# Optimization experiments

Hardware: AMD Instinct MI355X
Metric: run time of the kernel (lower is better)

## Reference

```python
import jax, jax.numpy as jnp
import numpy as np

QMIN, QMAX = -128.0, 127.0  # int8 fake-quant range for activations
BIAS_ZP = 128.0             # zero point for the uint8-stored quantized bias


def ste_fake_quant(x, scale, zp):
    # scaled fake-quantize: q = clip(round(x/s) + zp, qmin, qmax); deq = (q - zp) * s
    q = jnp.clip(jnp.round(x / scale) + zp, QMIN, QMAX)
    deq = (q - zp) * scale
    # straight-through estimator (matches torch fake_quantize semantics)
    return x + jax.lax.stop_gradient(deq - x)


def setup_inputs() -> dict:
    key = jax.random.key(0)
    ks = jax.random.split(key, 8)
    B, S, K, N, G = 8, 8192, 1024, 1024, 128
    NG = K // G  # groups per output channel
    x = jax.random.normal(ks[0], (B, S, K), dtype=jnp.float32)
    w_q = jax.random.randint(ks[1], (N, K), 0, 16, dtype=jnp.int32)          # int4 codes
    w_scale = jax.random.uniform(ks[2], (N, NG), dtype=jnp.float32) * 0.02 + 1e-3
    w_zp = jax.random.randint(ks[3], (N, NG), 0, 16, dtype=jnp.int32)
    bias_q = jax.random.randint(ks[4], (N,), 0, 256, dtype=jnp.int32)        # uint8 codes
    bias_scale = jax.random.uniform(ks[5], (N,), dtype=jnp.float32) * 0.01 + 1e-4
    in_scale = jax.random.uniform(ks[6], (1,), dtype=jnp.float32) * 0.02 + 0.01
    in_zp = jnp.zeros((1,), dtype=jnp.int32)
    out_scale = jax.random.uniform(ks[7], (1,), dtype=jnp.float32) * 0.2 + 0.05
    out_zp = jnp.zeros((1,), dtype=jnp.int32)
    return {"x": x, "w_q": w_q, "w_scale": w_scale, "w_zp": w_zp,
            "bias_q": bias_q, "bias_scale": bias_scale,
            "in_scale": in_scale, "in_zp": in_zp,
            "out_scale": out_scale, "out_zp": out_zp}


def reference(x, w_q, w_scale, w_zp, bias_q, bias_scale, in_scale, in_zp, out_scale, out_zp):
    dt = x.dtype
    N, K = w_q.shape
    NG = w_scale.shape[1]
    G = K // NG
    # group-wise weight dequantize: [N, K] -> [N, NG, G]
    wq = w_q.reshape(N, NG, G).astype(dt)
    W = ((wq - w_zp[:, :, None].astype(dt)) * w_scale[:, :, None].astype(dt)).reshape(N, K)
    # per-channel bias dequantize
    bias = (bias_q.astype(dt) - BIAS_ZP) * bias_scale.astype(dt)
    # per-tensor fake-quantize of the input activation
    xq = ste_fake_quant(x, in_scale.astype(dt), in_zp.astype(dt))
    # func_method: linear
    out = jnp.einsum('bsk,nk->bsn', xq, W) + bias
    # per-tensor fake-quantize of the output
    return ste_fake_quant(out, out_scale.astype(dt), out_zp.astype(dt))
```

## Files before the change

kernel.cpp:

```cpp
#include <hip/hip_runtime.h>
#include <hip/hip_bf16.h>
#include <stdint.h>

#define M_DIM 65536
#define K_DIM 1024
#define N_DIM 1024
#define NGRP  8

#define NIT 8

#define FB_BM 128
#define FB_BN 128
#define FB_BK 32
#define FB_NKT (K_DIM / FB_BK)

typedef float f32x4 __attribute__((ext_vector_type(4)));
typedef int   ix4   __attribute__((ext_vector_type(4)));
typedef __bf16 bf16x8 __attribute__((ext_vector_type(8)));

__global__ void prep_wd_kernel(const int* __restrict__ w_q,
                               const int* __restrict__ w_zp,
                               const int* __restrict__ bias_q,
                               const float* __restrict__ bias_scale,
                               int8_t* __restrict__ Wd,
                               float* __restrict__ bias_f) {
    const int n = blockIdx.x;
    const int t = threadIdx.x;
    const int k0 = t * 4;
    const int g = k0 >> 7;
    const int zp = w_zp[n * NGRP + g];
    const int4 wq = *reinterpret_cast<const int4*>(w_q + (size_t)n * K_DIM + k0);
    union { int u; int8_t b[4]; } pk;
    pk.b[0] = (int8_t)(wq.x - zp);
    pk.b[1] = (int8_t)(wq.y - zp);
    pk.b[2] = (int8_t)(wq.z - zp);
    pk.b[3] = (int8_t)(wq.w - zp);
    *reinterpret_cast<int*>(Wd + (size_t)n * K_DIM + k0) = pk.u;
    if (t == 0) bias_f[n] = ((float)bias_q[n] - 128.0f) * bias_scale[n];
}

__global__ __launch_bounds__(256) void prep_x8_kernel(
    const float* __restrict__ x,
    const float* __restrict__ in_scale_p, const int* __restrict__ in_zp_p,
    int8_t* __restrict__ Xq)
{
    const float s = in_scale_p[0];
    const float inv = 1.0f / s;
    const float zp = (float)in_zp_p[0];
    const size_t i = ((size_t)blockIdx.x * 256 + threadIdx.x) * 16;
    float vv[16];
#pragma unroll
    for (int c = 0; c < 4; ++c) {
        const float4 v = *reinterpret_cast<const float4*>(x + i + c * 4);
        vv[c * 4 + 0] = v.x; vv[c * 4 + 1] = v.y;
        vv[c * 4 + 2] = v.z; vv[c * 4 + 3] = v.w;
    }
    union { int4 u; int8_t b[16]; } pk;
#pragma unroll
    for (int e = 0; e < 16; ++e) {
        float q = rintf(vv[e] * inv) + zp;
        q = fminf(fmaxf(q, -128.0f), 127.0f);
        pk.b[e] = (int8_t)(q - zp);
    }
    *reinterpret_cast<int4*>(Xq + i) = pk.u;
}

__global__ __launch_bounds__(512, 2) void gemm256_i8_kernel(
    const int8_t* __restrict__ Xq,
    const int8_t* __restrict__ Wd,
    const float* __restrict__ w_scale,
    const float* __restrict__ bias_f,
    const float* __restrict__ in_scale_p,
    const float* __restrict__ out_scale_p, const int* __restrict__ out_zp_p,
    float* __restrict__ out)
{
    __shared__ __align__(16) int8_t LDS[8][16384];
    __shared__ float WS[NGRP * 256];

    const int t = threadIdx.x;
    const int bid = (blockIdx.x & 7) * 128 + (blockIdx.x >> 3);
    const int nt = bid & 3;
    const int mt = bid >> 2;
    const int m0 = mt * 256;
    const int n0 = nt * 256;

    const int wid = t >> 6;
    const int lane = t & 63;
    const int wr = wid >> 2, wc = wid & 3;
    const int lrow = lane & 15;
    const int kslot = lane >> 4;
    const int koff = ((kslot ^ ((lrow >> 1) & 3)) << 4);
    const int widoff = wid * 1024;

    char* ldsb = (char*)&LDS[0][0];
    const int8_t* Abase = Xq + (size_t)m0 * K_DIM;
    const int8_t* Bbase = Wd + (size_t)n0 * K_DIM;

    {
        const int nl = t >> 1;
        const int g4 = (t & 1) * 4;
        const float4 wv = *reinterpret_cast<const float4*>(
            w_scale + (size_t)(n0 + nl) * NGRP + g4);
        WS[(g4 + 0) * 256 + nl] = wv.x;
        WS[(g4 + 1) * 256 + nl] = wv.y;
        WS[(g4 + 2) * 256 + nl] = wv.z;
        WS[(g4 + 3) * 256 + nl] = wv.w;
    }
    asm volatile("s_waitcnt vmcnt(0) lgkmcnt(0)" ::: "memory");
    __builtin_amdgcn_s_barrier();
    __builtin_amdgcn_sched_barrier(0);

    auto stage = [&](int slot, const int8_t* panel, int kt64) {
        const int k0 = kt64 * 64;
#pragma unroll
        for (int j = 0; j < 2; ++j) {
            const int c = j * 512 + t;
            const int r = c >> 2;
            const int sl = (c & 3) ^ ((r >> 1) & 3);
            const int8_t* src = panel + (size_t)r * K_DIM + k0 + sl * 16;
            __builtin_amdgcn_global_load_lds(
                (const __attribute__((address_space(1))) void*)src,
                (__attribute__((address_space(3))) void*)(ldsb + slot * 16384 + j * 8192 + widoff),
                16, 0, 0);
        }
    };

    ix4 af[4], bfr[4];
    ix4 it0[4][4];
    f32x4 facc[8][4];
#pragma unroll
    for (int mi = 0; mi < 8; ++mi)
#pragma unroll
        for (int ni = 0; ni < 4; ++ni)
            facc[mi][ni] = (f32x4){0.f, 0.f, 0.f, 0.f};

#define RD_A(SLOT, MH)                                                        \
    _Pragma("unroll")                                                         \
    for (int i = 0; i < 4; ++i) {                                             \
        const int row = wr * 128 + ((MH) * 4 + i) * 16 + lrow;                \
        af[i] = *reinterpret_cast<const ix4*>(                                \
            ldsb + (SLOT) * 16384 + row * 64 + koff);                         \
    }
#define RD_B(SLOT)                                                            \
    _Pragma("unroll")                                                         \
    for (int i = 0; i < 4; ++i) {                                             \
        const int row = wc * 64 + i * 16 + lrow;                              \
        bfr[i] = *reinterpret_cast<const ix4*>(                               \
            ldsb + (SLOT) * 16384 + row * 64 + koff);                         \
    }
#define MFMA16_INIT                                                           \
    do { __builtin_amdgcn_s_setprio(1);                                       \
        _Pragma("unroll")                                                     \
        for (int mi = 0; mi < 4; ++mi)                                        \
            _Pragma("unroll")                                                 \
            for (int ni = 0; ni < 4; ++ni)                                    \
                it0[mi][ni] = __builtin_amdgcn_mfma_i32_16x16x64_i8(          \
                    af[mi], bfr[ni], (ix4){0, 0, 0, 0}, 0, 0, 0);             \
        __builtin_amdgcn_s_setprio(0); } while (0)
#define MFMA16_ACC                                                            \
    do { __builtin_amdgcn_s_setprio(1);                                       \
        _Pragma("unroll")                                                     \
        for (int mi = 0; mi < 4; ++mi)                                        \
            _Pragma("unroll")                                                 \
            for (int ni = 0; ni < 4; ++ni)                                    \
                it0[mi][ni] = __builtin_amdgcn_mfma_i32_16x16x64_i8(          \
                    af[mi], bfr[ni], it0[mi][ni], 0, 0, 0);                   \
        __builtin_amdgcn_s_setprio(0); } while (0)
#define CVT16(MH)                                                             \
    _Pragma("unroll")                                                         \
    for (int mi = 0; mi < 4; ++mi)                                            \
        _Pragma("unroll")                                                     \
        for (int ni = 0; ni < 4; ++ni)                                        \
            _Pragma("unroll")                                                 \
            for (int e = 0; e < 4; ++e)                                       \
                facc[(MH) * 4 + mi][ni][e] += wsv[ni] * (float)it0[mi][ni][e];
#define CLOSE                                                                 \
    do { __builtin_amdgcn_sched_barrier(0);                                   \
         __builtin_amdgcn_s_barrier();                                        \
         __builtin_amdgcn_sched_barrier(0); } while (0)
#define VM4 asm volatile("s_waitcnt vmcnt(4)" ::: "memory")
#define VM2 asm volatile("s_waitcnt vmcnt(2)" ::: "memory")
#define VM0 asm volatile("s_waitcnt vmcnt(0)" ::: "memory")

    stage(0, Abase, 0);
    stage(1, Bbase, 0);
    stage(2, Abase, 1);
    stage(3, Bbase, 1);
    VM4;
    CLOSE;

#pragma unroll 1
    for (int it = 0; it < NIT - 1; ++it) {
        const int b = (it & 1) * 4;
        const int nb = b ^ 4;
        const int tE = 2 * (it + 1);
        const int tO = tE + 1;
        const int nl = wc * 64 + lrow;

        float wsv[4];
#pragma unroll
        for (int ni = 0; ni < 4; ++ni) wsv[ni] = WS[it * 256 + nl + ni * 16];

        RD_B(b + 1); RD_A(b + 0, 0);
        stage(nb + 0, Abase, tE);
        MFMA16_INIT;
        VM2;
        CLOSE;
        RD_B(b + 3); RD_A(b + 2, 0);
        stage(nb + 1, Bbase, tE);
        MFMA16_ACC;
        CVT16(0);
        CLOSE;
        RD_B(b + 1); RD_A(b + 0, 1);
        stage(nb + 2, Abase, tO);
        MFMA16_INIT;
        CLOSE;
        RD_B(b + 3); RD_A(b + 2, 1);
        stage(nb + 3, Bbase, tO);
        MFMA16_ACC;
        CVT16(1);
        VM4;
        CLOSE;
    }

    {
        const int it = NIT - 1;
        const int b = 4;
        const int nl = wc * 64 + lrow;
        float wsv[4];
#pragma unroll
        for (int ni = 0; ni < 4; ++ni) wsv[ni] = WS[it * 256 + nl + ni * 16];

        RD_B(b + 1); RD_A(b + 0, 0);
        MFMA16_INIT;
        VM0;
        CLOSE;
        RD_B(b + 3); RD_A(b + 2, 0);
        MFMA16_ACC;
        CVT16(0);
        CLOSE;
        RD_B(b + 1); RD_A(b + 0, 1);
        MFMA16_INIT;
        CLOSE;
        RD_B(b + 3); RD_A(b + 2, 1);
        MFMA16_ACC;
        CVT16(1);
    }

#undef RD_A
#undef RD_B
#undef MFMA16_INIT
#undef MFMA16_ACC
#undef CVT16
#undef CLOSE
#undef VM4
#undef VM2
#undef VM0

    const float in_s  = in_scale_p[0];
    const float out_s = out_scale_p[0];
    const float out_inv = 1.0f / out_s;
    const float ozp = (float)out_zp_p[0];
    const int col = lane & 15;
    const int rgrp = lane >> 4;
#pragma unroll
    for (int ni = 0; ni < 4; ++ni) {
        const int n = n0 + wc * 64 + ni * 16 + col;
        const float bv = bias_f[n];
#pragma unroll
        for (int mi = 0; mi < 8; ++mi) {
#pragma unroll
            for (int j = 0; j < 4; ++j) {
                const int m = m0 + wr * 128 + mi * 16 + rgrp * 4 + j;
                float v = in_s * facc[mi][ni][j] + bv;
                float q = rintf(v * out_inv) + ozp;
                q = fminf(fmaxf(q, -128.0f), 127.0f);
                out[(size_t)m * N_DIM + n] = (q - ozp) * out_s;
            }
        }
    }
}

__global__ void prep_kernel(const int* __restrict__ w_q,
                            const float* __restrict__ w_scale,
                            const int* __restrict__ w_zp,
                            const int* __restrict__ bias_q,
                            const float* __restrict__ bias_scale,
                            __hip_bfloat16* __restrict__ Wb,
                            float* __restrict__ bias_f) {
    const int n = blockIdx.x;
    const int t = threadIdx.x;
    const int k0 = t * 4;
    const int g = k0 >> 7;
    const float s  = w_scale[n * NGRP + g];
    const float zp = (float)w_zp[n * NGRP + g];
    const int4 wq = *reinterpret_cast<const int4*>(w_q + (size_t)n * K_DIM + k0);
    union { ushort4 u; __hip_bfloat16 h[4]; } pk;
    pk.h[0] = __float2bfloat16(((float)wq.x - zp) * s);
    pk.h[1] = __float2bfloat16(((float)wq.y - zp) * s);
    pk.h[2] = __float2bfloat16(((float)wq.z - zp) * s);
    pk.h[3] = __float2bfloat16(((float)wq.w - zp) * s);
    *reinterpret_cast<ushort4*>(Wb + (size_t)n * K_DIM + k0) = pk.u;
    if (t == 0) bias_f[n] = ((float)bias_q[n] - 128.0f) * bias_scale[n];
}

__global__ __launch_bounds__(256) void gemm_fused_kernel(
    const float* __restrict__ x,
    const __hip_bfloat16* __restrict__ Wb,
    const float* __restrict__ bias_f,
    const float* __restrict__ in_scale_p, const int* __restrict__ in_zp_p,
    const float* __restrict__ out_scale_p, const int* __restrict__ out_zp_p,
    float* __restrict__ out)
{
    __shared__ __align__(16) __hip_bfloat16 As[2][FB_BM][FB_BK];
    __shared__ __align__(16) __hip_bfloat16 Bs[2][FB_BN][FB_BK];

    const int t = threadIdx.x;
    const int bid = blockIdx.x;
    const int nt = bid & 7;
    const int mt = bid >> 3;
    const int m0 = mt * FB_BM;
    const int n0 = nt * FB_BN;

    const int wid = t >> 6;
    const int lane = t & 63;
    const int wr = wid >> 1, wc = wid & 1;
    const int lrow = lane & 15;
    const int kslot = lane >> 4;

    const float in_s = in_scale_p[0];
    const float in_inv = 1.0f / in_s;
    const float izp = (float)in_zp_p[0];

    auto stageB = [&](int b, int kt) {
        const int k0 = kt * FB_BK;
#pragma unroll
        for (int j = 0; j < 2; ++j) {
            const int c = (wid * 2 + j) * 64 + lane;
            const int row = c >> 2;
            const int slot = c & 3;
            const __hip_bfloat16* src = Wb + (size_t)(n0 + row) * K_DIM + k0 + slot * 8;
            __builtin_amdgcn_global_load_lds(
                (const __attribute__((address_space(1))) void*)src,
                (__attribute__((address_space(3))) void*)((char*)&Bs[b][0][0] + (wid * 2 + j) * 1024),
                16, 0, 0);
        }
    };
    auto stageA = [&](int b, int kt) {
        const int k0 = kt * FB_BK;
#pragma unroll
        for (int i = 0; i < 4; ++i) {
            const int c = t + 256 * i;
            const int row = c >> 3;
            const int slot = c & 7;
            const float4 v = *reinterpret_cast<const float4*>(
                x + (size_t)(m0 + row) * K_DIM + k0 + slot * 4);
            float vv[4] = {v.x, v.y, v.z, v.w};
            union { ushort4 u; __hip_bfloat16 h[4]; } pk;
#pragma unroll
            for (int e = 0; e < 4; ++e) {
                float q = rintf(vv[e] * in_inv) + izp;
                q = fminf(fmaxf(q, -128.0f), 127.0f);
                pk.h[e] = __float2bfloat16((q - izp) * in_s);
            }
            *reinterpret_cast<ushort4*>(&As[b][row][slot * 4]) = pk.u;
        }
    };

    f32x4 acc[4][4];
#pragma unroll
    for (int mi = 0; mi < 4; ++mi)
#pragma unroll
        for (int ni = 0; ni < 4; ++ni)
            acc[mi][ni] = (f32x4){0.f, 0.f, 0.f, 0.f};

    stageB(0, 0);
    stageA(0, 0);
    __syncthreads();

    for (int kt = 0; kt < FB_NKT; ++kt) {
        const int buf = kt & 1;
        if (kt + 1 < FB_NKT) {
            stageB(buf ^ 1, kt + 1);
            stageA(buf ^ 1, kt + 1);
        }
        bf16x8 af[4], bfr[4];
#pragma unroll
        for (int mi = 0; mi < 4; ++mi)
            af[mi] = *reinterpret_cast<const bf16x8*>(&As[buf][wr * 64 + mi * 16 + lrow][kslot * 8]);
#pragma unroll
        for (int ni = 0; ni < 4; ++ni)
            bfr[ni] = *reinterpret_cast<const bf16x8*>(&Bs[buf][wc * 64 + ni * 16 + lrow][kslot * 8]);
#pragma unroll
        for (int mi = 0; mi < 4; ++mi)
#pragma unroll
            for (int ni = 0; ni < 4; ++ni)
                acc[mi][ni] = __builtin_amdgcn_mfma_f32_16x16x32_bf16(af[mi], bfr[ni], acc[mi][ni], 0, 0, 0);
        __syncthreads();
    }

    const float out_s = out_scale_p[0];
    const float out_inv = 1.0f / out_s;
    const float ozp = (float)out_zp_p[0];
    const int col = lane & 15;
    const int rgrp = lane >> 4;
#pragma unroll
    for (int ni = 0; ni < 4; ++ni) {
        const int n = n0 + wc * 64 + ni * 16 + col;
        const float bv = bias_f[n];
#pragma unroll
        for (int mi = 0; mi < 4; ++mi) {
#pragma unroll
            for (int j = 0; j < 4; ++j) {
                const int m = m0 + wr * 64 + mi * 16 + rgrp * 4 + j;
                float v = acc[mi][ni][j] + bv;
                float q = rintf(v * out_inv) + ozp;
                q = fminf(fmaxf(q, -128.0f), 127.0f);
                out[(size_t)m * N_DIM + n] = (q - ozp) * out_s;
            }
        }
    }
}

extern "C" void kernel_launch(void* const* d_in, const int* in_sizes, int n_in,
                              void* d_out, int out_size, void* d_ws, size_t ws_size,
                              hipStream_t stream) {
    const float* x          = (const float*)d_in[0];
    const int*   w_q        = (const int*)d_in[1];
    const float* w_scale    = (const float*)d_in[2];
    const int*   w_zp       = (const int*)d_in[3];
    const int*   bias_q     = (const int*)d_in[4];
    const float* bias_scale = (const float*)d_in[5];
    const float* in_scale   = (const float*)d_in[6];
    const int*   in_zp      = (const int*)d_in[7];
    const float* out_scale  = (const float*)d_in[8];
    const int*   out_zp     = (const int*)d_in[9];

    const size_t xq8_bytes = (size_t)M_DIM * K_DIM;
    const size_t wd_bytes  = (size_t)N_DIM * K_DIM;
    const size_t need = xq8_bytes + wd_bytes + N_DIM * sizeof(float);

    if (ws_size >= need) {
        int8_t* Xq8 = (int8_t*)d_ws;
        int8_t* Wd  = (int8_t*)((char*)d_ws + xq8_bytes);
        float* bias_f = (float*)((char*)d_ws + xq8_bytes + wd_bytes);

        prep_wd_kernel<<<N_DIM, 256, 0, stream>>>(w_q, w_zp, bias_q, bias_scale, Wd, bias_f);
        prep_x8_kernel<<<(int)(((size_t)M_DIM * K_DIM) / (256 * 16)), 256, 0, stream>>>(
            x, in_scale, in_zp, Xq8);

        const int grid = (M_DIM / 256) * (N_DIM / 256);
        gemm256_i8_kernel<<<grid, 512, 0, stream>>>(Xq8, Wd, w_scale, bias_f,
                                                    in_scale, out_scale, out_zp,
                                                    (float*)d_out);
    } else {
        __hip_bfloat16* Wb = (__hip_bfloat16*)d_ws;
        float* bias_f = (float*)((char*)d_ws + (size_t)N_DIM * K_DIM * sizeof(__hip_bfloat16));

        prep_kernel<<<N_DIM, 256, 0, stream>>>(w_q, w_scale, w_zp, bias_q, bias_scale, Wb, bias_f);
        const int grid = (M_DIM / FB_BM) * (N_DIM / FB_BN);
        gemm_fused_kernel<<<grid, 256, 0, stream>>>(x, Wb, bias_f, in_scale, in_zp,
                                                    out_scale, out_zp, (float*)d_out);
    }
}
```

Baseline: 229.8 us.

## Replace 256x256 hand-pipelined int8 GEMM with simpler 128x128 double-buffered kernel

Shrinks the int8 GEMM tile from 256x256 with 512 threads to 128x128 with 256 threads, aiming for three blocks per CU. It swaps the hand-scheduled eight-slot LDS pipeline (explicit vmcnt waits and priority hints) for a plain two-buffer loop synchronised with __syncthreads. Each 64-wide k-tile's int32 MFMA result is scaled into the float accumulator immediately, instead of accumulating two k-tiles per weight group first. This raises occupancy and simplifies scheduling, but doubles global operand traffic per output and doubles int-to-float conversion work.

```diff
diff --git a/kernel.cpp b/kernel.cpp
--- a/kernel.cpp
+++ b/kernel.cpp
@@ -7,7 +7,10 @@
 #define N_DIM 1024
 #define NGRP  8
 
-#define NIT 8
+#define T_BM 128
+#define T_BN 128
+#define T_BK 64
+#define T_NKT (K_DIM / T_BK)
 
 #define FB_BM 128
 #define FB_BN 128
@@ -65,7 +68,7 @@
     *reinterpret_cast<int4*>(Xq + i) = pk.u;
 }
 
-__global__ __launch_bounds__(512, 2) void gemm256_i8_kernel(
+__global__ __launch_bounds__(256, 3) void gemm128_i8_kernel(
     const int8_t* __restrict__ Xq,
     const int8_t* __restrict__ Wd,
     const float* __restrict__ w_scale,
@@ -74,25 +77,25 @@
     const float* __restrict__ out_scale_p, const int* __restrict__ out_zp_p,
     float* __restrict__ out)
 {
-    __shared__ __align__(16) int8_t LDS[8][16384];
-    __shared__ float WS[NGRP * 256];
+    __shared__ __align__(16) int8_t Abuf[2][T_BM * T_BK];
+    __shared__ __align__(16) int8_t Bbuf[2][T_BN * T_BK];
+    __shared__ float WS[NGRP * T_BN];
 
     const int t = threadIdx.x;
-    const int bid = (blockIdx.x & 7) * 128 + (blockIdx.x >> 3);
-    const int nt = bid & 3;
-    const int mt = bid >> 2;
-    const int m0 = mt * 256;
-    const int n0 = nt * 256;
+    const int bid = (blockIdx.x & 7) * 512 + (blockIdx.x >> 3);
+    const int nt = bid & 7;
+    const int mt = bid >> 3;
+    const int m0 = mt * T_BM;
+    const int n0 = nt * T_BN;
 
     const int wid = t >> 6;
     const int lane = t & 63;
-    const int wr = wid >> 2, wc = wid & 3;
+    const int wr = wid >> 1, wc = wid & 1;
     const int lrow = lane & 15;
     const int kslot = lane >> 4;
     const int koff = ((kslot ^ ((lrow >> 1) & 3)) << 4);
     const int widoff = wid * 1024;
 
-    char* ldsb = (char*)&LDS[0][0];
     const int8_t* Abase = Xq + (size_t)m0 * K_DIM;
     const int8_t* Bbase = Wd + (size_t)n0 * K_DIM;
 
@@ -101,161 +104,82 @@
         const int g4 = (t & 1) * 4;
         const float4 wv = *reinterpret_cast<const float4*>(
             w_scale + (size_t)(n0 + nl) * NGRP + g4);
-        WS[(g4 + 0) * 256 + nl] = wv.x;
-        WS[(g4 + 1) * 256 + nl] = wv.y;
-        WS[(g4 + 2) * 256 + nl] = wv.z;
-        WS[(g4 + 3) * 256 + nl] = wv.w;
-    }
-    asm volatile("s_waitcnt vmcnt(0) lgkmcnt(0)" ::: "memory");
-    __builtin_amdgcn_s_barrier();
-    __builtin_amdgcn_sched_barrier(0);
-
-    auto stage = [&](int slot, const int8_t* panel, int kt64) {
-        const int k0 = kt64 * 64;
+        WS[(g4 + 0) * T_BN + nl] = wv.x;
+        WS[(g4 + 1) * T_BN + nl] = wv.y;
+        WS[(g4 + 2) * T_BN + nl] = wv.z;
+        WS[(g4 + 3) * T_BN + nl] = wv.w;
+    }
+
+    auto stage = [&](int8_t* dst, const int8_t* panel, int kt) {
+        const int k0 = kt * T_BK;
 #pragma unroll
         for (int j = 0; j < 2; ++j) {
-            const int c = j * 512 + t;
+            const int c = j * 256 + t;
             const int r = c >> 2;
             const int sl = (c & 3) ^ ((r >> 1) & 3);
             const int8_t* src = panel + (size_t)r * K_DIM + k0 + sl * 16;
             __builtin_amdgcn_global_load_lds(
                 (const __attribute__((address_space(1))) void*)src,
-                (__attribute__((address_space(3))) void*)(ldsb + slot * 16384 + j * 8192 + widoff),
+                (__attribute__((address_space(3))) void*)(dst + j * 4096 + widoff),
                 16, 0, 0);
         }
     };
 
-    ix4 af[4], bfr[4];
-    ix4 it0[4][4];
-    f32x4 facc[8][4];
-#pragma unroll
-    for (int mi = 0; mi < 8; ++mi)
+    f32x4 facc[4][4];
+#pragma unroll
+    for (int mi = 0; mi < 4; ++mi)
 #pragma unroll
         for (int ni = 0; ni < 4; ++ni)
             facc[mi][ni] = (f32x4){0.f, 0.f, 0.f, 0.f};
 
-#define RD_A(SLOT, MH)                                                        \
-    _Pragma("unroll")                                                         \
-    for (int i = 0; i < 4; ++i) {                                             \
-        const int row = wr * 128 + ((MH) * 4 + i) * 16 + lrow;                \
-        af[i] = *reinterpret_cast<const ix4*>(                                \
-            ldsb + (SLOT) * 16384 + row * 64 + koff);                         \
-    }
-#define RD_B(SLOT)                                                            \
-    _Pragma("unroll")                                                         \
-    for (int i = 0; i < 4; ++i) {                                             \
-        const int row = wc * 64 + i * 16 + lrow;                              \
-        bfr[i] = *reinterpret_cast<const ix4*>(                               \
-            ldsb + (SLOT) * 16384 + row * 64 + koff);                         \
-    }
-#define MFMA16_INIT                                                           \
-    do { __builtin_amdgcn_s_setprio(1);                                       \
-        _Pragma("unroll")                                                     \
-        for (int mi = 0; mi < 4; ++mi)                                        \
-            _Pragma("unroll")                                                 \
-            for (int ni = 0; ni < 4; ++ni)                                    \
-                it0[mi][ni] = __builtin_amdgcn_mfma_i32_16x16x64_i8(          \
-                    af[mi], bfr[ni], (ix4){0, 0, 0, 0}, 0, 0, 0);             \
-        __builtin_amdgcn_s_setprio(0); } while (0)
-#define MFMA16_ACC                                                            \
-    do { __builtin_amdgcn_s_setprio(1);                                       \
-        _Pragma("unroll")                                                     \
-        for (int mi = 0; mi < 4; ++mi)                                        \
-            _Pragma("unroll")                                                 \
-            for (int ni = 0; ni < 4; ++ni)                                    \
-                it0[mi][ni] = __builtin_amdgcn_mfma_i32_16x16x64_i8(          \
-                    af[mi], bfr[ni], it0[mi][ni], 0, 0, 0);                   \
-        __builtin_amdgcn_s_setprio(0); } while (0)
-#define CVT16(MH)                                                             \
-    _Pragma("unroll")                                                         \
-    for (int mi = 0; mi < 4; ++mi)                                            \
-        _Pragma("unroll")                                                     \
-        for (int ni = 0; ni < 4; ++ni)                                        \
-            _Pragma("unroll")                                                 \
-            for (int e = 0; e < 4; ++e)                                       \
-                facc[(MH) * 4 + mi][ni][e] += wsv[ni] * (float)it0[mi][ni][e];
-#define CLOSE                                                                 \
-    do { __builtin_amdgcn_sched_barrier(0);                                   \
-         __builtin_amdgcn_s_barrier();                                        \
-         __builtin_amdgcn_sched_barrier(0); } while (0)
-#define VM4 asm volatile("s_waitcnt vmcnt(4)" ::: "memory")
-#define VM2 asm volatile("s_waitcnt vmcnt(2)" ::: "memory")
-#define VM0 asm volatile("s_waitcnt vmcnt(0)" ::: "memory")
-
-    stage(0, Abase, 0);
-    stage(1, Bbase, 0);
-    stage(2, Abase, 1);
-    stage(3, Bbase, 1);
-    VM4;
-    CLOSE;
-
+    stage(&Abuf[0][0], Abase, 0);
+    stage(&Bbuf[0][0], Bbase, 0);
+    __syncthreads();
+
+    int buf = 0;
 #pragma unroll 1
-    for (int it = 0; it < NIT - 1; ++it) {
-        const int b = (it & 1) * 4;
-        const int nb = b ^ 4;
-        const int tE = 2 * (it + 1);
-        const int tO = tE + 1;
-        const int nl = wc * 64 + lrow;
-
+    for (int kt = 0; kt < T_NKT; ++kt) {
+        if (kt + 1 < T_NKT) {
+            stage(&Abuf[buf ^ 1][0], Abase, kt + 1);
+            stage(&Bbuf[buf ^ 1][0], Bbase, kt + 1);
+        }
+
+        ix4 af[4], bfr[4];
+#pragma unroll
+        for (int i = 0; i < 4; ++i) {
+            const int arow = wr * 64 + i * 16 + lrow;
+            af[i] = *reinterpret_cast<const ix4*>(&Abuf[buf][arow * 64 + koff]);
+        }
+#pragma unroll
+        for (int i = 0; i < 4; ++i) {
+            const int brow = wc * 64 + i * 16 + lrow;
+            bfr[i] = *reinterpret_cast<const ix4*>(&Bbuf[buf][brow * 64 + koff]);
+        }
+
+        const int g = kt >> 1;
         float wsv[4];
 #pragma unroll
-        for (int ni = 0; ni < 4; ++ni) wsv[ni] = WS[it * 256 + nl + ni * 16];
-
-        RD_B(b + 1); RD_A(b + 0, 0);
-        stage(nb + 0, Abase, tE);
-        MFMA16_INIT;
-        VM2;
-        CLOSE;
-        RD_B(b + 3); RD_A(b + 2, 0);
-        stage(nb + 1, Bbase, tE);
-        MFMA16_ACC;
-        CVT16(0);
-        CLOSE;
-        RD_B(b + 1); RD_A(b + 0, 1);
-        stage(nb + 2, Abase, tO);
-        MFMA16_INIT;
-        CLOSE;
-        RD_B(b + 3); RD_A(b + 2, 1);
-        stage(nb + 3, Bbase, tO);
-        MFMA16_ACC;
-        CVT16(1);
-        VM4;
-        CLOSE;
-    }
-
-    {
-        const int it = NIT - 1;
-        const int b = 4;
-        const int nl = wc * 64 + lrow;
-        float wsv[4];
-#pragma unroll
-        for (int ni = 0; ni < 4; ++ni) wsv[ni] = WS[it * 256 + nl + ni * 16];
-
-        RD_B(b + 1); RD_A(b + 0, 0);
-        MFMA16_INIT;
-        VM0;
-        CLOSE;
-        RD_B(b + 3); RD_A(b + 2, 0);
-        MFMA16_ACC;
-        CVT16(0);
-        CLOSE;
-        RD_B(b + 1); RD_A(b + 0, 1);
-        MFMA16_INIT;
-        CLOSE;
-        RD_B(b + 3); RD_A(b + 2, 1);
-        MFMA16_ACC;
-        CVT16(1);
-    }
-
-#undef RD_A
-#undef RD_B
-#undef MFMA16_INIT
-#undef MFMA16_ACC
-#undef CVT16
-#undef CLOSE
-#undef VM4
-#undef VM2
-#undef VM0
+        for (int ni = 0; ni < 4; ++ni)
+            wsv[ni] = WS[g * T_BN + wc * 64 + ni * 16 + lrow];
+
+#pragma unroll
+        for (int mi = 0; mi < 4; ++mi) {
+            ix4 s0 = __builtin_amdgcn_mfma_i32_16x16x64_i8(af[mi], bfr[0], (ix4){0,0,0,0}, 0, 0, 0);
+            ix4 s1 = __builtin_amdgcn_mfma_i32_16x16x64_i8(af[mi], bfr[1], (ix4){0,0,0,0}, 0, 0, 0);
+            ix4 s2 = __builtin_amdgcn_mfma_i32_16x16x64_i8(af[mi], bfr[2], (ix4){0,0,0,0}, 0, 0, 0);
+            ix4 s3 = __builtin_amdgcn_mfma_i32_16x16x64_i8(af[mi], bfr[3], (ix4){0,0,0,0}, 0, 0, 0);
+#pragma unroll
+            for (int e = 0; e < 4; ++e) {
+                facc[mi][0][e] += wsv[0] * (float)s0[e];
+                facc[mi][1][e] += wsv[1] * (float)s1[e];
+                facc[mi][2][e] += wsv[2] * (float)s2[e];
+                facc[mi][3][e] += wsv[3] * (float)s3[e];
+            }
+        }
+
+        __syncthreads();
+        buf ^= 1;
+    }
 
     const float in_s  = in_scale_p[0];
     const float out_s = out_scale_p[0];
@@ -268,10 +192,10 @@
         const int n = n0 + wc * 64 + ni * 16 + col;
         const float bv = bias_f[n];
 #pragma unroll
-        for (int mi = 0; mi < 8; ++mi) {
+        for (int mi = 0; mi < 4; ++mi) {
 #pragma unroll
             for (int j = 0; j < 4; ++j) {
-                const int m = m0 + wr * 128 + mi * 16 + rgrp * 4 + j;
+                const int m = m0 + wr * 64 + mi * 16 + rgrp * 4 + j;
                 float v = in_s * facc[mi][ni][j] + bv;
                 float q = rintf(v * out_inv) + ozp;
                 q = fminf(fmaxf(q, -128.0f), 127.0f);
@@ -449,8 +373,8 @@
         prep_x8_kernel<<<(int)(((size_t)M_DIM * K_DIM) / (256 * 16)), 256, 0, stream>>>(
             x, in_scale, in_zp, Xq8);
 
-        const int grid = (M_DIM / 256) * (N_DIM / 256);
-        gemm256_i8_kernel<<<grid, 512, 0, stream>>>(Xq8, Wd, w_scale, bias_f,
+        const int grid = (M_DIM / T_BM) * (N_DIM / T_BN);
+        gemm128_i8_kernel<<<grid, 256, 0, stream>>>(Xq8, Wd, w_scale, bias_f,
                                                     in_scale, out_scale, out_zp,
                                                     (float*)d_out);
     } else {
```

Result: faster. 223.4 us (-2.8%).
